# Kernel optimization log

Hardware: AMD Instinct MI355X
Metric: run time of the kernel (lower is better)

Reference implementation:

```python
import jax, jax.numpy as jnp
import numpy as np

N, E, B = 50000, 600000, 64
C_IN, H, C_OUT, L = 128, 128, 64, 3
BN_EPS = 1e-5


def setup_inputs() -> dict:
    key = jax.random.key(0)
    ks = iter(jax.random.split(key, 40))

    def w(shape, fan_in):
        return jax.random.normal(next(ks), shape, jnp.float32) / np.sqrt(fan_in).astype(np.float32)

    return {
        "x": jax.random.normal(next(ks), (N, C_IN), jnp.float32),
        "edge_index": jax.random.randint(next(ks), (2, E), 0, N),
        "batch": jnp.sort(jax.random.randint(next(ks), (N,), 0, B)),
        # GINConv MLPs: Linear(in,h) -> BN -> ReLU -> Linear(h,h)   (stacked over L; C_IN == H)
        "convW1": w((L, C_IN, H), C_IN), "convb1": jnp.zeros((L, H), jnp.float32),
        "bn_g": jnp.ones((L, H), jnp.float32), "bn_b": jnp.zeros((L, H), jnp.float32),
        "convW2": w((L, H, H), H), "convb2": jnp.zeros((L, H), jnp.float32),
        # reconstruction head: Linear(h,h)-ReLU-Linear(h,h)-ReLU-Linear(h,4)-ReLU
        "recW1": w((H, H), H), "recb1": jnp.zeros((H,), jnp.float32),
        "recW2": w((H, H), H), "recb2": jnp.zeros((H,), jnp.float32),
        "recW3": w((H, 4), H), "recb3": jnp.zeros((4,), jnp.float32),
        # final MLP([h,h,out], norm=None): Linear(h,h)-ReLU-(dropout, eval=identity)-Linear(h,out)
        "mlpW1": w((H, H), H), "mlpb1": jnp.zeros((H,), jnp.float32),
        "mlpW2": w((H, C_OUT), H), "mlpb2": jnp.zeros((C_OUT,), jnp.float32),
    }


def reference(x, edge_index, batch, convW1, convb1, bn_g, bn_b, convW2, convb2,
              recW1, recb1, recW2, recb2, recW3, recb3, mlpW1, mlpb1, mlpW2, mlpb2):
    src, dst = edge_index[0], edge_index[1]
    for l in range(L):
        # GIN aggregation: out_i = nn((1+eps)*x_i + sum_{j->i} x_j), eps = 0
        agg = jax.ops.segment_sum(x[src], dst, num_segments=N)  # [N, d]
        h = (x + agg) @ convW1[l] + convb1[l]                   # [N, H]
        mu = h.mean(axis=0)
        var = jnp.var(h, axis=0)                                # biased, torch BN train mode
        h = bn_g[l] * (h - mu) * jax.lax.rsqrt(var + BN_EPS) + bn_b[l]
        h = jax.nn.relu(h) @ convW2[l] + convb2[l]
        x = jax.nn.relu(h)                                      # outer .relu() in forward
    # reconstruction branch on node features
    x_rec = jax.nn.relu(x @ recW1 + recb1)
    x_rec = jax.nn.relu(x_rec @ recW2 + recb2)
    x_rec = jax.nn.relu(x_rec @ recW3 + recb3)                  # [N, 4]
    # global_add_pool keyed by graph id
    pooled = jax.ops.segment_sum(x, batch, num_segments=B)      # [B, H]
    out = jax.nn.relu(pooled @ mlpW1 + mlpb1) @ mlpW2 + mlpb2   # [B, C_OUT]
    return (out, x_rec)
```

## Files before the change

### kernel.cpp

```cpp
#include <hip/hip_runtime.h>

#define NN 50000
#define EE 600000
#define BB 64
#define CH 128
#define LL 3
#define NGB 391
#define NSB 196
#define NPB 392

typedef unsigned short u16;
typedef unsigned int u32;
typedef short s16x8 __attribute__((ext_vector_type(8)));
typedef float f32x4 __attribute__((ext_vector_type(4)));

__device__ __forceinline__ u16 f2b(float f) {
    u32 x = __float_as_uint(f);
    return (u16)((x + 0x7FFFu + ((x >> 16) & 1u)) >> 16);
}
__device__ __forceinline__ float b2f(u16 u) {
    return __uint_as_float(((u32)u) << 16);
}

__global__ __launch_bounds__(256) void k_prep(
    const float* __restrict__ x, u16* __restrict__ x16,
    const float* __restrict__ cW1, const float* __restrict__ cW2,
    const float* __restrict__ rW1, const float* __restrict__ rW2,
    const float* __restrict__ rW3, u16* __restrict__ Wt,
    int* __restrict__ deg, float* __restrict__ pooled,
    float* __restrict__ gstats) {
    int gid = blockIdx.x * 256 + threadIdx.x;

    long base = (long)gid * 8;
    if (base < (long)NN * CH) {
        float4 f0 = *(const float4*)(x + base);
        float4 f1 = *(const float4*)(x + base + 4);
        union { u16 pk[8]; uint4 v; } uu;
        uu.pk[0] = f2b(f0.x); uu.pk[1] = f2b(f0.y);
        uu.pk[2] = f2b(f0.z); uu.pk[3] = f2b(f0.w);
        uu.pk[4] = f2b(f1.x); uu.pk[5] = f2b(f1.y);
        uu.pk[6] = f2b(f1.z); uu.pk[7] = f2b(f1.w);
        *(uint4*)(x16 + base) = uu.v;
    }
    if (gid < 8 * 16384) {
        int slot = gid >> 14;
        int wi = gid & 16383;
        int k = wi >> 7, n = wi & 127;
        const float* src = slot < 3 ? cW1 + slot * 16384
                         : slot < 6 ? cW2 + (slot - 3) * 16384
                         : slot == 6 ? rW1 : rW2;
        Wt[slot * 16384 + n * 128 + k] = f2b(src[wi]);
    } else if (gid < 9 * 16384) {
        int j = gid - 8 * 16384;
        int n = j >> 7, k = j & 127;
        Wt[8 * 16384 + j] = (n < 4) ? f2b(rW3[k * 4 + n]) : (u16)0;
    }
    if (gid < NN) deg[gid] = 0;
    int j2 = gid - NN;
    if (j2 >= 0 && j2 < BB * CH) pooled[j2] = 0.f;
    int k2 = j2 - BB * CH;
    if (k2 >= 0 && k2 < 3 * 256) gstats[k2] = 0.f;
}

__global__ __launch_bounds__(256) void k_count(const int* __restrict__ ei,
                                               int* __restrict__ deg) {
    int e = blockIdx.x * 256 + threadIdx.x;
    if (e < EE) atomicAdd(&deg[ei[EE + e]], 1);
}

__global__ __launch_bounds__(256) void k_scanA(const int* __restrict__ deg,
                                               int* __restrict__ bsum) {
    __shared__ int sm[256];
    int i = blockIdx.x * 256 + threadIdx.x;
    sm[threadIdx.x] = (i < NN) ? deg[i] : 0;
    __syncthreads();
    for (int off = 128; off > 0; off >>= 1) {
        if (threadIdx.x < off) sm[threadIdx.x] += sm[threadIdx.x + off];
        __syncthreads();
    }
    if (threadIdx.x == 0) bsum[blockIdx.x] = sm[0];
}

__global__ __launch_bounds__(256) void k_scanB(const int* __restrict__ deg,
                                               const int* __restrict__ bsum,
                                               int* __restrict__ rowptr,
                                               int* __restrict__ cur) {
    __shared__ int sb[256], sd[256];
    int t = threadIdx.x;
    sb[t] = (t < NSB) ? bsum[t] : 0;
    __syncthreads();
    for (int off = 1; off < 256; off <<= 1) {
        int v = (t >= off) ? sb[t - off] : 0;
        __syncthreads();
        sb[t] += v;
        __syncthreads();
    }
    int blockOff = (blockIdx.x == 0) ? 0 : sb[blockIdx.x - 1];
    int i = blockIdx.x * 256 + t;
    int d = (i < NN) ? deg[i] : 0;
    sd[t] = d;
    __syncthreads();
    for (int off = 1; off < 256; off <<= 1) {
        int v = (t >= off) ? sd[t - off] : 0;
        __syncthreads();
        sd[t] += v;
        __syncthreads();
    }
    int excl = blockOff + sd[t] - d;
    if (i < NN) { rowptr[i] = excl; cur[i] = excl; }
    if (i == NN - 1) rowptr[NN] = excl + d;
}

__global__ __launch_bounds__(256) void k_fill(const int* __restrict__ ei,
                                              int* __restrict__ cur,
                                              int* __restrict__ perm) {
    int e = blockIdx.x * 256 + threadIdx.x;
    if (e < EE) {
        int dst = ei[EE + e];
        int idx = atomicAdd(&cur[dst], 1);
        perm[idx] = ei[e];
    }
}

__global__ __launch_bounds__(256) void k_gather(const u16* __restrict__ x,
                                                const int* __restrict__ rowptr,
                                                const int* __restrict__ perm,
                                                u16* __restrict__ y) {
    int dst = blockIdx.x * 16 + (threadIdx.x >> 4);
    int lane = threadIdx.x & 15;
    int co = lane * 8;
    int beg = rowptr[dst], end = rowptr[dst + 1];
    union { u16 pk[8]; uint4 v; } uu;
    uu.v = *(const uint4*)(x + (long)dst * CH + co);
    float a[8], b[8], c[8], d[8];
#pragma unroll
    for (int j = 0; j < 8; ++j) { a[j] = b2f(uu.pk[j]); b[j] = 0.f; c[j] = 0.f; d[j] = 0.f; }
    int e = beg;
    for (; e + 3 < end; e += 4) {
        int s0 = perm[e], s1 = perm[e + 1], s2 = perm[e + 2], s3 = perm[e + 3];
        union { u16 pk[8]; uint4 v; } v0, v1, v2, v3;
        v0.v = *(const uint4*)(x + (long)s0 * CH + co);
        v1.v = *(const uint4*)(x + (long)s1 * CH + co);
        v2.v = *(const uint4*)(x + (long)s2 * CH + co);
        v3.v = *(const uint4*)(x + (long)s3 * CH + co);
#pragma unroll
        for (int j = 0; j < 8; ++j) {
            a[j] += b2f(v0.pk[j]); b[j] += b2f(v1.pk[j]);
            c[j] += b2f(v2.pk[j]); d[j] += b2f(v3.pk[j]);
        }
    }
    for (; e < end; ++e) {
        int s0 = perm[e];
        union { u16 pk[8]; uint4 v; } v0;
        v0.v = *(const uint4*)(x + (long)s0 * CH + co);
#pragma unroll
        for (int j = 0; j < 8; ++j) a[j] += b2f(v0.pk[j]);
    }
    union { u16 pk[8]; uint4 v; } ov;
#pragma unroll
    for (int j = 0; j < 8; ++j) ov.pk[j] = f2b((a[j] + b[j]) + (c[j] + d[j]));
    *(uint4*)(y + (long)dst * CH + co) = ov.v;
}

__device__ __forceinline__ void stageB8(const u16* __restrict__ Wt, u16* sB,
                                        int s, int rr) {
#pragma unroll
    for (int it = 0; it < 8; ++it) {
        int n = it * 16 + rr;
        uint4 u = *(const uint4*)(Wt + n * CH + 8 * s);
        *(uint4*)(&sB[n * CH + ((s ^ (n & 15)) * 8)]) = u;
    }
}

__device__ __forceinline__ void mfma8(const u16* sA, const u16* sB,
                                      f32x4 acc[2][8], int wv, int quad, int l16) {
    f32x4 z = {0.f, 0.f, 0.f, 0.f};
#pragma unroll
    for (int m = 0; m < 2; ++m)
#pragma unroll
        for (int t = 0; t < 8; ++t) acc[m][t] = z;
    const u16* pa0 = sA + (wv * 32 + l16) * CH;
    const u16* pa1 = pa0 + 16 * CH;
#pragma unroll
    for (int kc = 0; kc < 4; ++kc) {
        int off = (((kc << 2) | quad) ^ l16) << 3;
        s16x8 a0 = *(const s16x8*)(pa0 + off);
        s16x8 a1 = *(const s16x8*)(pa1 + off);
#pragma unroll
        for (int t = 0; t < 8; ++t) {
            s16x8 bfr = *(const s16x8*)(sB + (t * 16 + l16) * CH + off);
            acc[0][t] = __builtin_amdgcn_mfma_f32_16x16x32_bf16(a0, bfr, acc[0][t], 0, 0, 0);
            acc[1][t] = __builtin_amdgcn_mfma_f32_16x16x32_bf16(a1, bfr, acc[1][t], 0, 0, 0);
        }
    }
}

__device__ __forceinline__ void biasrelu(f32x4 acc[2][8],
                                         const float* __restrict__ bias, int l16) {
#pragma unroll
    for (int t = 0; t < 8; ++t) {
        float bv = bias[t * 16 + l16];
#pragma unroll
        for (int m = 0; m < 2; ++m)
#pragma unroll
            for (int r = 0; r < 4; ++r)
                acc[m][t][r] = fmaxf(acc[m][t][r] + bv, 0.f);
    }
}

__device__ __forceinline__ void restage(const f32x4 acc[2][8], u16* sA,
                                        int wv, int quad, int l16) {
#pragma unroll
    for (int t = 0; t < 8; ++t) {
        int chunk = (t << 1) | (l16 >> 3);
        int o7 = l16 & 7;
#pragma unroll
        for (int m = 0; m < 2; ++m)
#pragma unroll
            for (int r = 0; r < 4; ++r) {
                int lr = wv * 32 + m * 16 + quad * 4 + r;
                sA[lr * CH + ((chunk ^ (lr & 15)) << 3) + o7] = f2b(acc[m][t][r]);
            }
    }
}

__global__ __launch_bounds__(256, 2) void k_gemm1(
    u16* __restrict__ hy, const u16* __restrict__ Wt, int layer,
    const float* __restrict__ cb1, float* __restrict__ gstats) {
    __shared__ u16 sA[128 * CH];
    __shared__ u16 sB[128 * CH];
    const int tid = threadIdx.x;
    const int s = tid & 15, rr = tid >> 4;
    const int r0 = blockIdx.x * 128;
    const int lane = tid & 63, wv = tid >> 6, quad = lane >> 4, l16 = lane & 15;

    stageB8(Wt + layer * 16384, sB, s, rr);
#pragma unroll
    for (int it = 0; it < 8; ++it) {
        int lr = it * 16 + rr, gr = r0 + lr;
        union { u16 pk[8]; uint4 v; } uu;
        if (gr < NN) {
            uu.v = *(const uint4*)(hy + (long)gr * CH + 8 * s);
        } else {
#pragma unroll
            for (int j = 0; j < 8; ++j) uu.pk[j] = 0;
        }
        *(uint4*)(&sA[lr * CH + ((s ^ (lr & 15)) * 8)]) = uu.v;
    }
    __syncthreads();
    f32x4 acc[2][8];
    mfma8(sA, sB, acc, wv, quad, l16);

    float ss[8], qq[8];
#pragma unroll
    for (int t = 0; t < 8; ++t) {
        float bv = cb1[t * 16 + l16];
        ss[t] = 0.f; qq[t] = 0.f;
#pragma unroll
        for (int m = 0; m < 2; ++m) {
            int rbase = r0 + wv * 32 + m * 16 + quad * 4;
#pragma unroll
            for (int r = 0; r < 4; ++r) {
                float v = acc[m][t][r] + bv;
                acc[m][t][r] = v;
                if (rbase + r < NN) { ss[t] += v; qq[t] += v * v; }
            }
        }
    }
#pragma unroll
    for (int t = 0; t < 8; ++t) {
        ss[t] += __shfl_xor(ss[t], 16);
        ss[t] += __shfl_xor(ss[t], 32);
        qq[t] += __shfl_xor(qq[t], 16);
        qq[t] += __shfl_xor(qq[t], 32);
    }
    float* red = (float*)sA;
    __syncthreads();
    if (lane < 16) {
#pragma unroll
        for (int t = 0; t < 8; ++t) {
            red[wv * 256 + t * 16 + l16] = ss[t];
            red[wv * 256 + 128 + t * 16 + l16] = qq[t];
        }
    }
    __syncthreads();
    unsafeAtomicAdd(&gstats[tid],
                    red[tid] + red[256 + tid] + red[512 + tid] + red[768 + tid]);

#pragma unroll
    for (int t = 0; t < 8; ++t) {
        int col = t * 16 + l16;
#pragma unroll
        for (int m = 0; m < 2; ++m)
#pragma unroll
            for (int r = 0; r < 4; ++r) {
                int row = r0 + wv * 32 + m * 16 + quad * 4 + r;
                if (row < NN) hy[(long)row * CH + col] = f2b(acc[m][t][r]);
            }
    }
}

template <bool LAST>
__global__ __launch_bounds__(256, 2) void k_gemm2(
    const u16* __restrict__ h16, const u16* __restrict__ Wt, int layer,
    const float* __restrict__ g, const float* __restrict__ bbeta,
    const float* __restrict__ gstats, const float* __restrict__ cb2,
    u16* __restrict__ xc,
    const float* __restrict__ rb1, const float* __restrict__ rb2,
    const float* __restrict__ rb3, float* __restrict__ x_rec) {
    __shared__ u16 sA[128 * CH];
    __shared__ u16 sB[128 * CH];
    __shared__ float snorm[256];
    const int tid = threadIdx.x;
    const int s = tid & 15, rr = tid >> 4;
    const int r0 = blockIdx.x * 128;
    const int lane = tid & 63, wv = tid >> 6, quad = lane >> 4, l16 = lane & 15;

    if (tid < 128) {
        float sum = gstats[tid];
        float sq = gstats[128 + tid];
        float mu = sum / (float)NN;
        float var = sq / (float)NN - mu * mu;
        float sc = g[tid] * rsqrtf(var + 1e-5f);
        snorm[tid] = sc;
        snorm[128 + tid] = bbeta[tid] - mu * sc;
    }
    stageB8(Wt + (3 + layer) * 16384, sB, s, rr);
    __syncthreads();

#pragma unroll
    for (int it = 0; it < 8; ++it) {
        int lr = it * 16 + rr, gr = r0 + lr;
        union { u16 pk[8]; uint4 v; } uu;
        if (gr < NN) {
            uu.v = *(const uint4*)(h16 + (long)gr * CH + 8 * s);
#pragma unroll
            for (int j = 0; j < 8; ++j) {
                int c = 8 * s + j;
                float v = fmaxf(b2f(uu.pk[j]) * snorm[c] + snorm[128 + c], 0.f);
                uu.pk[j] = f2b(v);
            }
        } else {
#pragma unroll
            for (int j = 0; j < 8; ++j) uu.pk[j] = 0;
        }
        *(uint4*)(&sA[lr * CH + ((s ^ (lr & 15)) * 8)]) = uu.v;
    }
    __syncthreads();
    f32x4 acc[2][8];
    mfma8(sA, sB, acc, wv, quad, l16);
    biasrelu(acc, cb2, l16);
#pragma unroll
    for (int t = 0; t < 8; ++t) {
        int col = t * 16 + l16;
#pragma unroll
        for (int m = 0; m < 2; ++m)
#pragma unroll
            for (int r = 0; r < 4; ++r) {
                int row = r0 + wv * 32 + m * 16 + quad * 4 + r;
                if (row < NN) xc[(long)row * CH + col] = f2b(acc[m][t][r]);
            }
    }

    if constexpr (LAST) {
        __syncthreads();
        restage(acc, sA, wv, quad, l16);
        stageB8(Wt + 6 * 16384, sB, s, rr);
        __syncthreads();
        mfma8(sA, sB, acc, wv, quad, l16);
        biasrelu(acc, rb1, l16);
        __syncthreads();
        restage(acc, sA, wv, quad, l16);
        stageB8(Wt + 7 * 16384, sB, s, rr);
        __syncthreads();
        mfma8(sA, sB, acc, wv, quad, l16);
        biasrelu(acc, rb2, l16);
        __syncthreads();
        restage(acc, sA, wv, quad, l16);
        {
            int n = rr;
            uint4 u = *(const uint4*)(Wt + 8 * 16384 + n * CH + 8 * s);
            *(uint4*)(&sB[n * CH + ((s ^ (n & 15)) * 8)]) = u;
        }
        __syncthreads();
        f32x4 a4[2];
        a4[0] = (f32x4){0.f, 0.f, 0.f, 0.f};
        a4[1] = (f32x4){0.f, 0.f, 0.f, 0.f};
        const u16* pa0 = sA + (wv * 32 + l16) * CH;
        const u16* pa1 = pa0 + 16 * CH;
#pragma unroll
        for (int kc = 0; kc < 4; ++kc) {
            int off = (((kc << 2) | quad) ^ l16) << 3;
            s16x8 a0 = *(const s16x8*)(pa0 + off);
            s16x8 a1 = *(const s16x8*)(pa1 + off);
            s16x8 bfr = *(const s16x8*)(sB + l16 * CH + off);
            a4[0] = __builtin_amdgcn_mfma_f32_16x16x32_bf16(a0, bfr, a4[0], 0, 0, 0);
            a4[1] = __builtin_amdgcn_mfma_f32_16x16x32_bf16(a1, bfr, a4[1], 0, 0, 0);
        }
        if (l16 < 4) {
            float bv = rb3[l16];
#pragma unroll
            for (int m = 0; m < 2; ++m)
#pragma unroll
                for (int r = 0; r < 4; ++r) {
                    int row = r0 + wv * 32 + m * 16 + quad * 4 + r;
                    if (row < NN) x_rec[(long)row * 4 + l16] = fmaxf(a4[m][r] + bv, 0.f);
                }
        }
    }
}

__global__ __launch_bounds__(256) void k_pool(const u16* __restrict__ x,
                                              const int* __restrict__ batch,
                                              float* __restrict__ pooled) {
    int r0 = blockIdx.x * 128;
    if (r0 >= NN) return;
    int rend = r0 + 128 < NN ? r0 + 128 : NN;
    int c = threadIdx.x & 127;
    int half = threadIdx.x >> 7;
    int r = r0 + half;
    if (r >= rend) return;
    int g = batch[r];
    float s = 0.f;
    for (; r < rend; r += 2) {
        int gg = batch[r];
        if (gg != g) {
            unsafeAtomicAdd(pooled + g * CH + c, s);
            s = 0.f;
            g = gg;
        }
        s += b2f(x[(long)r * CH + c]);
    }
    unsafeAtomicAdd(pooled + g * CH + c, s);
}

__global__ __launch_bounds__(128) void k_mlp(const float* __restrict__ pooled,
                                             const float* __restrict__ W1,
                                             const float* __restrict__ b1,
                                             const float* __restrict__ W2,
                                             const float* __restrict__ b2,
                                             float* __restrict__ out) {
    __shared__ float p[128], t1[128];
    int b = blockIdx.x, t = threadIdx.x;
    p[t] = pooled[b * CH + t];
    __syncthreads();
    float acc = b1[t];
    for (int k = 0; k < 128; ++k) acc += p[k] * W1[k * 128 + t];
    t1[t] = fmaxf(acc, 0.f);
    __syncthreads();
    if (t < 64) {
        float o = b2[t];
        for (int k = 0; k < 128; ++k) o += t1[k] * W2[k * 64 + t];
        out[b * 64 + t] = o;
    }
}

extern "C" void kernel_launch(void* const* d_in, const int* in_sizes, int n_in,
                              void* d_out, int out_size, void* d_ws, size_t ws_size,
                              hipStream_t stream) {
    const float* x_in   = (const float*)d_in[0];
    const int*   ei     = (const int*)d_in[1];
    const int*   batch  = (const int*)d_in[2];
    const float* convW1 = (const float*)d_in[3];
    const float* convb1 = (const float*)d_in[4];
    const float* bn_g   = (const float*)d_in[5];
    const float* bn_b   = (const float*)d_in[6];
    const float* convW2 = (const float*)d_in[7];
    const float* convb2 = (const float*)d_in[8];
    const float* recW1  = (const float*)d_in[9];
    const float* recb1  = (const float*)d_in[10];
    const float* recW2  = (const float*)d_in[11];
    const float* recb2  = (const float*)d_in[12];
    const float* recW3  = (const float*)d_in[13];
    const float* recb3  = (const float*)d_in[14];
    const float* mlpW1  = (const float*)d_in[15];
    const float* mlpb1  = (const float*)d_in[16];
    const float* mlpW2  = (const float*)d_in[17];
    const float* mlpb2  = (const float*)d_in[18];

    float* out   = (float*)d_out;
    float* x_rec = out + 4096;

    char* w = (char*)d_ws;
    u16*   x16    = (u16*)w;    w += (size_t)NN * CH * 2;
    u16*   y16    = (u16*)w;    w += (size_t)NN * CH * 2;
    u16*   xc     = (u16*)w;    w += (size_t)NN * CH * 2;
    u16*   Wt     = (u16*)w;    w += (size_t)9 * 16384 * 2;
    float* gstats = (float*)w;  w += (size_t)3 * 256 * 4;
    float* pooled = (float*)w;  w += (size_t)BB * CH * 4;
    int*   deg    = (int*)w;    w += (size_t)NN * 4;
    int*   bsum   = (int*)w;    w += (size_t)NSB * 4;
    int*   rowptr = (int*)w;    w += (size_t)(NN + 1) * 4;
    int*   cur    = (int*)w;    w += (size_t)NN * 4;
    int*   perm   = (int*)w;    w += (size_t)EE * 4;

    dim3 b256(256), b128(128);

    k_prep<<<3125, b256, 0, stream>>>(x_in, x16, convW1, convW2, recW1, recW2,
                                      recW3, Wt, deg, pooled, gstats);
    k_count<<<2344, b256, 0, stream>>>(ei, deg);
    k_scanA<<<NSB, b256, 0, stream>>>(deg, bsum);
    k_scanB<<<NSB, b256, 0, stream>>>(deg, bsum, rowptr, cur);
    k_fill<<<2344, b256, 0, stream>>>(ei, cur, perm);

    const u16* cur_x = x16;
    for (int l = 0; l < LL; ++l) {
        k_gather<<<3125, b256, 0, stream>>>(cur_x, rowptr, perm, y16);
        k_gemm1<<<NGB, b256, 0, stream>>>(y16, Wt, l, convb1 + l * 128,
                                          gstats + l * 256);
        if (l < LL - 1)
            k_gemm2<false><<<NGB, b256, 0, stream>>>(
                y16, Wt, l, bn_g + l * 128, bn_b + l * 128, gstats + l * 256,
                convb2 + l * 128, xc, recb1, recb2, recb3, x_rec);
        else
            k_gemm2<true><<<NGB, b256, 0, stream>>>(
                y16, Wt, l, bn_g + l * 128, bn_b + l * 128, gstats + l * 256,
                convb2 + l * 128, xc, recb1, recb2, recb3, x_rec);
        cur_x = xc;
    }
    k_pool<<<NPB, b256, 0, stream>>>(xc, batch, pooled);
    k_mlp<<<64, b128, 0, stream>>>(pooled, mlpW1, mlpb1, mlpW2, mlpb2, out);
}
```

Measured before the change: 376.8 us.

## Store node features in 32-column chunked layout and compress edge indices to u16

Node features are now stored as four column-chunks of 32 features each. The gather kernel assigns each block to one chunk and 64 destination nodes, so the rows it gathers at random come from a smaller working set. The CSR source-index array is stored as 16-bit values, which halves index traffic; this works because node ids fit under 65536. gemm1 now writes to a separate h16 buffer because its chunked input cannot be overwritten in place. The risk is that each gathered row is only 64 bytes, which may use cache lines less efficiently, and the four chunks are interleaved across consecutive blocks.

```diff
diff --git a/kernel.cpp b/kernel.cpp
--- a/kernel.cpp
+++ b/kernel.cpp
@@ -6,6 +6,7 @@
 #define CH 128
 #define LL 3
 #define NGB 391
+#define NGA 3128
 #define NSB 196
 #define NPB 392
 
@@ -13,6 +14,7 @@
 typedef unsigned int u32;
 typedef short s16x8 __attribute__((ext_vector_type(8)));
 typedef float f32x4 __attribute__((ext_vector_type(4)));
+
 
 __device__ __forceinline__ u16 f2b(float f) {
     u32 x = __float_as_uint(f);
@@ -40,7 +42,9 @@
         uu.pk[2] = f2b(f0.z); uu.pk[3] = f2b(f0.w);
         uu.pk[4] = f2b(f1.x); uu.pk[5] = f2b(f1.y);
         uu.pk[6] = f2b(f1.z); uu.pk[7] = f2b(f1.w);
-        *(uint4*)(x16 + base) = uu.v;
+        long row = base >> 7;
+        int col = (int)(base & 127);
+        *(uint4*)(x16 + ((size_t)(col >> 5) * NN + row) * 32 + (col & 31)) = uu.v;
     }
     if (gid < 8 * 16384) {
         int slot = gid >> 14;
@@ -113,25 +117,28 @@
 
 __global__ __launch_bounds__(256) void k_fill(const int* __restrict__ ei,
                                               int* __restrict__ cur,
-                                              int* __restrict__ perm) {
+                                              u16* __restrict__ perm) {
     int e = blockIdx.x * 256 + threadIdx.x;
     if (e < EE) {
         int dst = ei[EE + e];
         int idx = atomicAdd(&cur[dst], 1);
-        perm[idx] = ei[e];
+        perm[idx] = (u16)ei[e];
     }
 }
 
 __global__ __launch_bounds__(256) void k_gather(const u16* __restrict__ x,
                                                 const int* __restrict__ rowptr,
-                                                const int* __restrict__ perm,
+                                                const u16* __restrict__ perm,
                                                 u16* __restrict__ y) {
-    int dst = blockIdx.x * 16 + (threadIdx.x >> 4);
-    int lane = threadIdx.x & 15;
-    int co = lane * 8;
+    int chunk = blockIdx.x & 3;
+    int rb = blockIdx.x >> 2;
+    int dst = rb * 64 + (threadIdx.x >> 2);
+    if (dst >= NN) return;
+    int gl = threadIdx.x & 3;
+    const u16* xb = x + (size_t)chunk * NN * 32 + gl * 8;
     int beg = rowptr[dst], end = rowptr[dst + 1];
     union { u16 pk[8]; uint4 v; } uu;
-    uu.v = *(const uint4*)(x + (long)dst * CH + co);
+    uu.v = *(const uint4*)(xb + (size_t)dst * 32);
     float a[8], b[8], c[8], d[8];
 #pragma unroll
     for (int j = 0; j < 8; ++j) { a[j] = b2f(uu.pk[j]); b[j] = 0.f; c[j] = 0.f; d[j] = 0.f; }
@@ -139,10 +146,10 @@
     for (; e + 3 < end; e += 4) {
         int s0 = perm[e], s1 = perm[e + 1], s2 = perm[e + 2], s3 = perm[e + 3];
         union { u16 pk[8]; uint4 v; } v0, v1, v2, v3;
-        v0.v = *(const uint4*)(x + (long)s0 * CH + co);
-        v1.v = *(const uint4*)(x + (long)s1 * CH + co);
-        v2.v = *(const uint4*)(x + (long)s2 * CH + co);
-        v3.v = *(const uint4*)(x + (long)s3 * CH + co);
+        v0.v = *(const uint4*)(xb + (size_t)s0 * 32);
+        v1.v = *(const uint4*)(xb + (size_t)s1 * 32);
+        v2.v = *(const uint4*)(xb + (size_t)s2 * 32);
+        v3.v = *(const uint4*)(xb + (size_t)s3 * 32);
 #pragma unroll
         for (int j = 0; j < 8; ++j) {
             a[j] += b2f(v0.pk[j]); b[j] += b2f(v1.pk[j]);
@@ -152,14 +159,14 @@
     for (; e < end; ++e) {
         int s0 = perm[e];
         union { u16 pk[8]; uint4 v; } v0;
-        v0.v = *(const uint4*)(x + (long)s0 * CH + co);
+        v0.v = *(const uint4*)(xb + (size_t)s0 * 32);
 #pragma unroll
         for (int j = 0; j < 8; ++j) a[j] += b2f(v0.pk[j]);
     }
     union { u16 pk[8]; uint4 v; } ov;
 #pragma unroll
     for (int j = 0; j < 8; ++j) ov.pk[j] = f2b((a[j] + b[j]) + (c[j] + d[j]));
-    *(uint4*)(y + (long)dst * CH + co) = ov.v;
+    *(uint4*)(y + (size_t)chunk * NN * 32 + (size_t)dst * 32 + gl * 8) = ov.v;
 }
 
 __device__ __forceinline__ void stageB8(const u16* __restrict__ Wt, u16* sB,
@@ -225,8 +232,9 @@
 }
 
 __global__ __launch_bounds__(256, 2) void k_gemm1(
-    u16* __restrict__ hy, const u16* __restrict__ Wt, int layer,
-    const float* __restrict__ cb1, float* __restrict__ gstats) {
+    const u16* __restrict__ y16, const u16* __restrict__ Wt, int layer,
+    const float* __restrict__ cb1, float* __restrict__ gstats,
+    u16* __restrict__ h16) {
     __shared__ u16 sA[128 * CH];
     __shared__ u16 sB[128 * CH];
     const int tid = threadIdx.x;
@@ -240,7 +248,7 @@
         int lr = it * 16 + rr, gr = r0 + lr;
         union { u16 pk[8]; uint4 v; } uu;
         if (gr < NN) {
-            uu.v = *(const uint4*)(hy + (long)gr * CH + 8 * s);
+            uu.v = *(const uint4*)(y16 + ((size_t)(s >> 2) * NN + gr) * 32 + (s & 3) * 8);
         } else {
 #pragma unroll
             for (int j = 0; j < 8; ++j) uu.pk[j] = 0;
@@ -295,7 +303,7 @@
 #pragma unroll
             for (int r = 0; r < 4; ++r) {
                 int row = r0 + wv * 32 + m * 16 + quad * 4 + r;
-                if (row < NN) hy[(long)row * CH + col] = f2b(acc[m][t][r]);
+                if (row < NN) h16[(long)row * CH + col] = f2b(acc[m][t][r]);
             }
     }
 }
@@ -352,13 +360,13 @@
     biasrelu(acc, cb2, l16);
 #pragma unroll
     for (int t = 0; t < 8; ++t) {
-        int col = t * 16 + l16;
+        u16* xcp = xc + (size_t)(t >> 1) * NN * 32 + (t & 1) * 16 + l16;
 #pragma unroll
         for (int m = 0; m < 2; ++m)
 #pragma unroll
             for (int r = 0; r < 4; ++r) {
                 int row = r0 + wv * 32 + m * 16 + quad * 4 + r;
-                if (row < NN) xc[(long)row * CH + col] = f2b(acc[m][t][r]);
+                if (row < NN) xcp[(size_t)row * 32] = f2b(acc[m][t][r]);
             }
     }
 
@@ -420,6 +428,7 @@
     int half = threadIdx.x >> 7;
     int r = r0 + half;
     if (r >= rend) return;
+    const u16* xp = x + (size_t)(c >> 5) * NN * 32 + (c & 31);
     int g = batch[r];
     float s = 0.f;
     for (; r < rend; r += 2) {
@@ -429,7 +438,7 @@
             s = 0.f;
             g = gg;
         }
-        s += b2f(x[(long)r * CH + c]);
+        s += b2f(xp[(size_t)r * 32]);
     }
     unsafeAtomicAdd(pooled + g * CH + c, s);
 }
@@ -484,6 +493,7 @@
     char* w = (char*)d_ws;
     u16*   x16    = (u16*)w;    w += (size_t)NN * CH * 2;
     u16*   y16    = (u16*)w;    w += (size_t)NN * CH * 2;
+    u16*   h16    = (u16*)w;    w += (size_t)NN * CH * 2;
     u16*   xc     = (u16*)w;    w += (size_t)NN * CH * 2;
     u16*   Wt     = (u16*)w;    w += (size_t)9 * 16384 * 2;
     float* gstats = (float*)w;  w += (size_t)3 * 256 * 4;
@@ -492,7 +502,7 @@
     int*   bsum   = (int*)w;    w += (size_t)NSB * 4;
     int*   rowptr = (int*)w;    w += (size_t)(NN + 1) * 4;
     int*   cur    = (int*)w;    w += (size_t)NN * 4;
-    int*   perm   = (int*)w;    w += (size_t)EE * 4;
+    u16*   perm   = (u16*)w;    w += (size_t)EE * 2;
 
     dim3 b256(256), b128(128);
 
@@ -505,16 +515,16 @@
 
     const u16* cur_x = x16;
     for (int l = 0; l < LL; ++l) {
-        k_gather<<<3125, b256, 0, stream>>>(cur_x, rowptr, perm, y16);
+        k_gather<<<NGA, b256, 0, stream>>>(cur_x, rowptr, perm, y16);
         k_gemm1<<<NGB, b256, 0, stream>>>(y16, Wt, l, convb1 + l * 128,
-                                          gstats + l * 256);
+                                          gstats + l * 256, h16);
         if (l < LL - 1)
             k_gemm2<false><<<NGB, b256, 0, stream>>>(
-                y16, Wt, l, bn_g + l * 128, bn_b + l * 128, gstats + l * 256,
+                h16, Wt, l, bn_g + l * 128, bn_b + l * 128, gstats + l * 256,
                 convb2 + l * 128, xc, recb1, recb2, recb3, x_rec);
         else
             k_gemm2<true><<<NGB, b256, 0, stream>>>(
-                y16, Wt, l, bn_g + l * 128, bn_b + l * 128, gstats + l * 256,
+                h16, Wt, l, bn_g + l * 128, bn_b + l * 128, gstats + l * 256,
                 convb2 + l * 128, xc, recb1, recb2, recb3, x_rec);
         cur_x = xc;
     }
```

Result: no change. 371.8 us, median of 2 (-1.3%).
